# Kernel tuning notes

Measured on AMD Instinct MI355X. Metric: run time of the kernel, lower is better.

## Reference

```python
import jax, jax.numpy as jnp
import numpy as np

MAX_DISPLACEMENT = 4  # matches init_kwargs
EPS = 1e-12  # torch F.normalize clamp


def _l2_normalize(x):
    # L2 normalize over channel dim (axis=1), matching torch.nn.functional.normalize
    n = jnp.sqrt(jnp.sum(x * x, axis=1, keepdims=True))
    return x / jnp.maximum(n, EPS)


def setup_inputs() -> dict:
    key = jax.random.key(0)
    k1, k2 = jax.random.split(key)
    B, C, H, W = 16, 256, 64, 64
    fA = jax.random.normal(k1, (B, C, H, W), dtype=jnp.float32)
    fB = jax.random.normal(k2, (B, C, H, W), dtype=jnp.float32)
    return {"fA": fA, "fB": fB}


def reference(fA, fB):
    d = MAX_DISPLACEMENT
    B, C, H, W = fA.shape
    fAn = _l2_normalize(fA)
    fBn = _l2_normalize(fB)
    # zero-pad fB by d (matches F.unfold padding=d), then take shifted windows.
    fBp = jnp.pad(fBn, ((0, 0), (0, 0), (d, d), (d, d)))
    outs = []
    # Fixed structural loop over (2d+1)^2 = 81 displacements (row-major ky, kx,
    # matching F.unfold's kernel-position ordering). No huge patch tensor is
    # materialized; each term is a channel dot-product of fA with shifted fB.
    for dy in range(2 * d + 1):
        for dx in range(2 * d + 1):
            shifted = jax.lax.dynamic_slice(
                fBp, (0, 0, dy, dx), (B, C, H, W))
            outs.append(jnp.sum(fAn * shifted, axis=1))  # (B, H, W)
    return jnp.stack(outs, axis=1)  # (B, (2d+1)^2, H, W)
```

## Files before the change

### kernel.cpp

```cpp
#include <hip/hip_runtime.h>
#include <hip/hip_bf16.h>
#include <math.h>

typedef short short8 __attribute__((ext_vector_type(8)));
typedef float f32x16 __attribute__((ext_vector_type(16)));

#define BB 16
#define CC 256
#define HH 64
#define WW 64
#define HWX 4096
#define DD 4
#define KD 9
#define KK 81
#define NSLOT 10

#define RAW_BAR() do { \
    asm volatile("s_waitcnt lgkmcnt(0)" ::: "memory"); \
    __builtin_amdgcn_s_barrier(); \
} while (0)

__device__ __forceinline__ short bf16c(float x) {
    __hip_bfloat16 h = __float2bfloat16(x);
    return *reinterpret_cast<short*>(&h);
}

__device__ __forceinline__ int lds_byte(int w, int c) {
    return (w * 512 + c * 2) ^ ((w & 31) << 4);
}

__device__ __forceinline__ void b_issue16(const float* __restrict__ row,
                                          int c0, int l, float* v) {
    #pragma unroll
    for (int j = 0; j < 16; ++j)
        v[j] = row[(size_t)(c0 + j) * HWX + l];
}

__device__ __forceinline__ float b_commit16(const float* v, unsigned short* bufp,
                                            int c0, int l) {
    float ss = 0.f;
    #pragma unroll
    for (int j = 0; j < 16; ++j) ss += v[j] * v[j];
    #pragma unroll
    for (int h = 0; h < 2; ++h) {
        short8 st;
        #pragma unroll
        for (int j = 0; j < 8; ++j) st[j] = bf16c(v[h * 8 + j]);
        *(short8*)((char*)bufp + lds_byte(l, c0 + h * 8)) = st;
    }
    return ss;
}

__global__ __launch_bounds__(512) void corr_mfma(
    const float* __restrict__ fA, const float* __restrict__ fB,
    float* __restrict__ out)
{
    __shared__ __attribute__((aligned(16))) unsigned short buf[WW * CC];
    __shared__ float part[2][8 * WW];
    __shared__ float invA_ls[2][WW];

    const int bid = blockIdx.x;
    const int swzb = (bid & 7) * 64 + (bid >> 3);
    const int b = swzb >> 5, jr = swzb & 31;
    const int h0 = 2 * jr;

    const int tid = threadIdx.x;
    const int l = tid & 63;
    const int wvu = __builtin_amdgcn_readfirstlane(tid >> 6);
    const int g = wvu >> 2;
    const int q = wvu & 3;
    const int hg = h0 + g;
    const int ti = q >> 1, tj = q & 1;
    const int ml = l & 31, kg = l >> 5;
    const int m = ti * 32 + ml;
    const int n = tj * 32 + ml;

    short8 afr[16];
    #pragma unroll
    for (int t = 0; t < 2; ++t) {
        {
            const float* Ar = fA + (size_t)b * CC * HWX + (size_t)(h0 + t) * WW;
            float ss = 0.f;
            #pragma unroll
            for (int r2 = 0; r2 < 4; ++r2) {
                const int c = wvu * 32 + r2 * 8;
                float v[8]; short8 st;
                #pragma unroll
                for (int j = 0; j < 8; ++j) v[j] = Ar[(size_t)(c + j) * HWX + l];
                #pragma unroll
                for (int j = 0; j < 8; ++j) ss += v[j] * v[j];
                #pragma unroll
                for (int j = 0; j < 8; ++j) st[j] = bf16c(v[j]);
                *(short8*)((char*)buf + lds_byte(l, c)) = st;
            }
            part[1][wvu * 64 + l] = ss;
        }
        __syncthreads();
        if (tid < WW) {
            float s = 0.f;
            #pragma unroll
            for (int qq = 0; qq < 8; ++qq) s += part[1][qq * 64 + tid];
            invA_ls[t][tid] = 1.f / fmaxf(sqrtf(s), 1e-12f);
        }
        if (g == t) {
            #pragma unroll
            for (int s = 0; s < 16; ++s)
                afr[s] = *(const short8*)((const char*)buf + lds_byte(m, s * 16 + kg * 8));
        }
        __syncthreads();
        if (g == t) {
            const float iam = invA_ls[t][m];
            #pragma unroll
            for (int s = 0; s < 16; ++s) {
                short8 tt = afr[s];
                #pragma unroll
                for (int j = 0; j < 8; ++j) {
                    union { unsigned u; float f; } uu;
                    uu.u = ((unsigned)(unsigned short)tt[j]) << 16;
                    tt[j] = bf16c(uu.f * iam);
                }
                afr[s] = tt;
            }
        }
    }

    const float* fBb = fB + (size_t)b * CC * HWX;
    {
        const int hb0 = h0 - DD;
        if ((unsigned)hb0 < HH) {
            const float* row = fBb + (size_t)hb0 * WW;
            float v[16];
            b_issue16(row, wvu * 32, l, v);
            float ss = b_commit16(v, buf, wvu * 32, l);
            b_issue16(row, wvu * 32 + 16, l, v);
            ss += b_commit16(v, buf, wvu * 32 + 16, l);
            part[0][wvu * 64 + l] = ss;
        }
    }
    __syncthreads();

    for (int r = 0; r < NSLOT; ++r) {
        const int hb = h0 - DD + r;
        const bool vcur = (unsigned)hb < HH;
        const bool vnext = (r + 1 < NSLOT) && ((unsigned)(hb + 1) < HH);
        const int dy = r - g;
        const bool dyv = (dy >= 0 && dy < KD);
        const bool comp = dyv && vcur;
        const float* nrow = fBb + (size_t)(hb + 1) * WW;
        float* ob = out + (((size_t)b * KK + dy * KD) * HH + hg) * WW;

        float va[16], vb[16];
        if (vnext) {
            b_issue16(nrow, wvu * 32, l, va);
            b_issue16(nrow, wvu * 32 + 16, l, vb);
        }

        if (comp) {
            f32x16 acc;
            #pragma unroll
            for (int i = 0; i < 16; ++i) acc[i] = 0.f;
            __builtin_amdgcn_s_setprio(1);
            #pragma unroll
            for (int s = 0; s < 16; ++s) {
                short8 bfr = *(const short8*)((const char*)buf + lds_byte(n, s * 16 + kg * 8));
                acc = __builtin_amdgcn_mfma_f32_32x32x16_bf16(afr[s], bfr, acc, 0, 0, 0);
            }
            __builtin_amdgcn_s_setprio(0);
            float sB = 0.f;
            #pragma unroll
            for (int qq = 0; qq < 8; ++qq) sB += part[r & 1][qq * 64 + n];
            const float ibn = 1.f / fmaxf(sqrtf(sB), 1e-12f);
            #pragma unroll
            for (int rr = 0; rr < 16; ++rr) {
                const int w = ti * 32 + (rr & 3) + 8 * (rr >> 2) + 4 * kg;
                const int dx = n - w + 4;
                if (dx >= 0 && dx < KD)
                    ob[(size_t)dx * HWX + w] = acc[rr] * ibn;
            }
            if (q == 3) {
                int i = -1;
                if (l < 10) i = l;
                else if (l >= 16 && l < 26) i = l - 16;
                if (i >= 0) {
                    const int wz0 = (i < 4) ? 0 : (i < 7) ? 1 : (i < 9) ? 2 : 3;
                    const int dx0 = i - ((wz0 == 0) ? 0 : (wz0 == 1) ? 4 : (wz0 == 2) ? 7 : 9);
                    const int wz = (l < 10) ? wz0 : 63 - wz0;
                    const int dxz = (l < 10) ? dx0 : 8 - dx0;
                    ob[(size_t)dxz * HWX + wz] = 0.f;
                }
            }
        } else if (dyv) {
            for (int i = q * 64 + l; i < KD * WW; i += 256)
                ob[(size_t)(i >> 6) * HWX + (i & 63)] = 0.f;
        }

        RAW_BAR();
        if (vnext) {
            float ssn = b_commit16(va, buf, wvu * 32, l);
            ssn += b_commit16(vb, buf, wvu * 32 + 16, l);
            part[(r + 1) & 1][wvu * 64 + l] = ssn;
        }
        RAW_BAR();
    }
}

extern "C" void kernel_launch(void* const* d_in, const int* in_sizes, int n_in,
                              void* d_out, int out_size, void* d_ws, size_t ws_size,
                              hipStream_t stream) {
    const float* fA = (const float*)d_in[0];
    const float* fB = (const float*)d_in[1];
    float* outp = (float*)d_out;
    corr_mfma<<<dim3(BB * HH / 2), 512, 0, stream>>>(fA, fB, outp);
}
```

Measured before the change: 62.28 us.

## Process one output row per 256-thread block instead of two rows per 512-thread block

Each block now handles a single output row h with 4 waves, so the grid doubles and each block stages 9 fB rows instead of 10. Sharing the fB row buffer between two output rows is dropped, which raises total fB global reads by about 1.8x. In exchange there are no idle waves on the edge slots and the blocks are smaller, which may help occupancy. Half of the next fB row is now loaded synchronously after the barrier rather than prefetched, which exposes global load latency inside each iteration.

```diff
diff --git a/kernel.cpp b/kernel.cpp
--- a/kernel.cpp
+++ b/kernel.cpp
@@ -13,7 +13,7 @@
 #define DD 4
 #define KD 9
 #define KK 81
-#define NSLOT 10
+#define NSLOT 9
 
 #define RAW_BAR() do { \
     asm volatile("s_waitcnt lgkmcnt(0)" ::: "memory"); \
@@ -51,108 +51,96 @@
     return ss;
 }
 
-__global__ __launch_bounds__(512) void corr_mfma(
+__global__ __launch_bounds__(256) void corr_mfma(
     const float* __restrict__ fA, const float* __restrict__ fB,
     float* __restrict__ out)
 {
     __shared__ __attribute__((aligned(16))) unsigned short buf[WW * CC];
-    __shared__ float part[2][8 * WW];
-    __shared__ float invA_ls[2][WW];
+    __shared__ float part[2][4 * WW];
+    __shared__ float invA_ls[WW];
 
     const int bid = blockIdx.x;
-    const int swzb = (bid & 7) * 64 + (bid >> 3);
-    const int b = swzb >> 5, jr = swzb & 31;
-    const int h0 = 2 * jr;
+    const int swz = (bid & 7) * 128 + (bid >> 3);
+    const int b = swz >> 6, h = swz & 63;
 
     const int tid = threadIdx.x;
     const int l = tid & 63;
-    const int wvu = __builtin_amdgcn_readfirstlane(tid >> 6);
-    const int g = wvu >> 2;
-    const int q = wvu & 3;
-    const int hg = h0 + g;
+    const int q = __builtin_amdgcn_readfirstlane(tid >> 6);
     const int ti = q >> 1, tj = q & 1;
     const int ml = l & 31, kg = l >> 5;
     const int m = ti * 32 + ml;
     const int n = tj * 32 + ml;
 
+    const float* Abase = fA + (size_t)b * CC * HWX + (size_t)h * WW;
+    {
+        float ss = 0.f;
+        #pragma unroll
+        for (int r = 0; r < 8; ++r) {
+            const int c = q * 64 + r * 8;
+            float v[8]; short8 st;
+            #pragma unroll
+            for (int j = 0; j < 8; ++j) v[j] = Abase[(size_t)(c + j) * HWX + l];
+            #pragma unroll
+            for (int j = 0; j < 8; ++j) ss += v[j] * v[j];
+            #pragma unroll
+            for (int j = 0; j < 8; ++j) st[j] = bf16c(v[j]);
+            *(short8*)((char*)buf + lds_byte(l, c)) = st;
+        }
+        part[1][q * 64 + l] = ss;
+    }
+    __syncthreads();
+    if (tid < WW) {
+        float s = part[1][tid] + part[1][64 + tid] + part[1][128 + tid] + part[1][192 + tid];
+        invA_ls[tid] = 1.f / fmaxf(sqrtf(s), 1e-12f);
+    }
     short8 afr[16];
     #pragma unroll
-    for (int t = 0; t < 2; ++t) {
-        {
-            const float* Ar = fA + (size_t)b * CC * HWX + (size_t)(h0 + t) * WW;
-            float ss = 0.f;
-            #pragma unroll
-            for (int r2 = 0; r2 < 4; ++r2) {
-                const int c = wvu * 32 + r2 * 8;
-                float v[8]; short8 st;
-                #pragma unroll
-                for (int j = 0; j < 8; ++j) v[j] = Ar[(size_t)(c + j) * HWX + l];
-                #pragma unroll
-                for (int j = 0; j < 8; ++j) ss += v[j] * v[j];
-                #pragma unroll
-                for (int j = 0; j < 8; ++j) st[j] = bf16c(v[j]);
-                *(short8*)((char*)buf + lds_byte(l, c)) = st;
-            }
-            part[1][wvu * 64 + l] = ss;
-        }
-        __syncthreads();
-        if (tid < WW) {
-            float s = 0.f;
-            #pragma unroll
-            for (int qq = 0; qq < 8; ++qq) s += part[1][qq * 64 + tid];
-            invA_ls[t][tid] = 1.f / fmaxf(sqrtf(s), 1e-12f);
-        }
-        if (g == t) {
-            #pragma unroll
-            for (int s = 0; s < 16; ++s)
-                afr[s] = *(const short8*)((const char*)buf + lds_byte(m, s * 16 + kg * 8));
-        }
-        __syncthreads();
-        if (g == t) {
-            const float iam = invA_ls[t][m];
-            #pragma unroll
-            for (int s = 0; s < 16; ++s) {
-                short8 tt = afr[s];
-                #pragma unroll
-                for (int j = 0; j < 8; ++j) {
-                    union { unsigned u; float f; } uu;
-                    uu.u = ((unsigned)(unsigned short)tt[j]) << 16;
-                    tt[j] = bf16c(uu.f * iam);
-                }
-                afr[s] = tt;
-            }
-        }
-    }
-
+    for (int s = 0; s < 16; ++s)
+        afr[s] = *(const short8*)((const char*)buf + lds_byte(m, s * 16 + kg * 8));
+    __syncthreads();
+    {
+        const float iam = invA_ls[m];
+        #pragma unroll
+        for (int s = 0; s < 16; ++s) {
+            short8 t = afr[s];
+            #pragma unroll
+            for (int j = 0; j < 8; ++j) {
+                union { unsigned u; float f; } uu;
+                uu.u = ((unsigned)(unsigned short)t[j]) << 16;
+                t[j] = bf16c(uu.f * iam);
+            }
+            afr[s] = t;
+        }
+    }
     const float* fBb = fB + (size_t)b * CC * HWX;
     {
-        const int hb0 = h0 - DD;
+        const int hb0 = h - DD;
         if ((unsigned)hb0 < HH) {
             const float* row = fBb + (size_t)hb0 * WW;
             float v[16];
-            b_issue16(row, wvu * 32, l, v);
-            float ss = b_commit16(v, buf, wvu * 32, l);
-            b_issue16(row, wvu * 32 + 16, l, v);
-            ss += b_commit16(v, buf, wvu * 32 + 16, l);
-            part[0][wvu * 64 + l] = ss;
+            float ss = 0.f;
+            #pragma unroll
+            for (int ch = 0; ch < 4; ++ch) {
+                b_issue16(row, q * 64 + ch * 16, l, v);
+                ss += b_commit16(v, buf, q * 64 + ch * 16, l);
+            }
+            part[0][q * 64 + l] = ss;
         }
     }
     __syncthreads();
 
     for (int r = 0; r < NSLOT; ++r) {
-        const int hb = h0 - DD + r;
-        const bool vcur = (unsigned)hb < HH;
+        const int p = r & 1;
+        const int hb = h - DD + r;
+        const bool comp = (unsigned)hb < HH;
         const bool vnext = (r + 1 < NSLOT) && ((unsigned)(hb + 1) < HH);
-        const int dy = r - g;
-        const bool dyv = (dy >= 0 && dy < KD);
-        const bool comp = dyv && vcur;
         const float* nrow = fBb + (size_t)(hb + 1) * WW;
-        float* ob = out + (((size_t)b * KK + dy * KD) * HH + hg) * WW;
+        float* ob = out + (((size_t)b * KK + (size_t)r * KD) * HH + h) * WW;
 
         float va[16], vb[16];
         if (vnext) {
-            b_issue16(nrow, wvu * 32, l, va);
-            b_issue16(nrow, wvu * 32 + 16, l, vb);
+            b_issue16(nrow, q * 64, l, va);
+            b_issue16(nrow, q * 64 + 16, l, vb);
         }
 
         if (comp) {
@@ -166,9 +154,7 @@
                 acc = __builtin_amdgcn_mfma_f32_32x32x16_bf16(afr[s], bfr, acc, 0, 0, 0);
             }
             __builtin_amdgcn_s_setprio(0);
-            float sB = 0.f;
-            #pragma unroll
-            for (int qq = 0; qq < 8; ++qq) sB += part[r & 1][qq * 64 + n];
+            float sB = part[p][n] + part[p][64 + n] + part[p][128 + n] + part[p][192 + n];
             const float ibn = 1.f / fmaxf(sqrtf(sB), 1e-12f);
             #pragma unroll
             for (int rr = 0; rr < 16; ++rr) {
@@ -189,16 +175,21 @@
                     ob[(size_t)dxz * HWX + wz] = 0.f;
                 }
             }
-        } else if (dyv) {
+        } else {
             for (int i = q * 64 + l; i < KD * WW; i += 256)
                 ob[(size_t)(i >> 6) * HWX + (i & 63)] = 0.f;
         }
 
         RAW_BAR();
         if (vnext) {
-            float ssn = b_commit16(va, buf, wvu * 32, l);
-            ssn += b_commit16(vb, buf, wvu * 32 + 16, l);
-            part[(r + 1) & 1][wvu * 64 + l] = ssn;
+            float ssn = b_commit16(va, buf, q * 64, l);
+            ssn += b_commit16(vb, buf, q * 64 + 16, l);
+            float vc[16], vd[16];
+            b_issue16(nrow, q * 64 + 32, l, vc);
+            b_issue16(nrow, q * 64 + 48, l, vd);
+            ssn += b_commit16(vc, buf, q * 64 + 32, l);
+            ssn += b_commit16(vd, buf, q * 64 + 48, l);
+            part[(r + 1) & 1][q * 64 + l] = ssn;
         }
         RAW_BAR();
     }
@@ -210,5 +201,5 @@
     const float* fA = (const float*)d_in[0];
     const float* fB = (const float*)d_in[1];
     float* outp = (float*)d_out;
-    corr_mfma<<<dim3(BB * HH / 2), 512, 0, stream>>>(fA, fB, outp);
-}
+    corr_mfma<<<dim3(BB * HH), 256, 0, stream>>>(fA, fB, outp);
+}
```

Result: slower. 71.97 us (+15.6%).
